# Kernel tuning notes

Measured on AMD Instinct MI355X. Metric: run time of the kernel, lower is better.

The kernel has to match this reference:

```python
import jax, jax.numpy as jnp
import numpy as np

N, E, F, H, L = 100000, 1200000, 64, 64, 4


def setup_inputs() -> dict:
    key = jax.random.key(0)
    ks = jax.random.split(key, 24)
    s = 1.0 / np.sqrt(H)
    x = jax.random.normal(ks[0], (N, F), dtype=jnp.float32)
    edge_index = jax.random.randint(ks[1], (2, E), 0, N, dtype=jnp.int32)
    W1 = jax.random.normal(ks[2], (F, H), jnp.float32) / np.sqrt(F)
    b1 = jnp.zeros((H,), jnp.float32)
    W2 = jax.random.normal(ks[3], (H, H), jnp.float32) * s
    b2 = jnp.zeros((H,), jnp.float32)
    # stacked per-direction (2: fw, bw) per-layer (L) conv params
    def mk(k):
        return jax.random.normal(k, (2, L, H, H), jnp.float32) * s
    gWk, gWq, gWv, gWs = mk(ks[4]), mk(ks[5]), mk(ks[6]), mk(ks[7])
    gbk = jnp.zeros((2, L, H), jnp.float32)
    gbq = jnp.zeros((2, L, H), jnp.float32)
    gbv = jnp.zeros((2, L, H), jnp.float32)
    gb = jnp.zeros((2, L, H), jnp.float32)
    Wsc = jax.random.normal(ks[8], (2 * H, 1), jnp.float32) / np.sqrt(2 * H)
    bsc = jnp.zeros((1,), jnp.float32)
    return dict(x=x, edge_index=edge_index, W1=W1, b1=b1, W2=W2, b2=b2,
                gWk=gWk, gbk=gbk, gWq=gWq, gbq=gbq, gWv=gWv, gbv=gbv,
                gWs=gWs, gb=gb, Wsc=Wsc, bsc=bsc)


def _res_gated_conv(h, src, dst, Wk, bk, Wq, bq, Wv, bv, Ws, b):
    # PyG ResGatedGraphConv: out_i = h_i @ Ws + b + sum_{(j->i)} sigmoid(k_i + q_j) * v_j
    k = h @ Wk + bk            # [N,H]
    q = h @ Wq + bq            # [N,H]
    v = h @ Wv + bv            # [N,H]
    eta = jax.nn.sigmoid(k[dst] + q[src])          # [E,H] per-edge gate
    agg = jax.ops.segment_sum(eta * v[src], dst, num_segments=h.shape[0])
    return agg + h @ Ws + b


def reference(x, edge_index, W1, b1, W2, b2, gWk, gbk, gWq, gbq, gWv, gbv, gWs, gb, Wsc, bsc):
    h = jax.nn.relu(x @ W1 + b1) @ W2 + b2
    src, dst = edge_index[0], edge_index[1]
    # forward direction: messages source -> target (aggregate at dst)
    h_fw = h
    for l in range(L):
        h_fw = _res_gated_conv(h_fw, src, dst, gWk[0, l], gbk[0, l], gWq[0, l], gbq[0, l],
                               gWv[0, l], gbv[0, l], gWs[0, l], gb[0, l])
    # backward direction: flow 'target_to_source' (aggregate at src)
    h_bw = h
    for l in range(L):
        h_bw = _res_gated_conv(h_bw, dst, src, gWk[1, l], gbk[1, l], gWq[1, l], gbq[1, l],
                               gWv[1, l], gbv[1, l], gWs[1, l], gb[1, l])
    score = jnp.concatenate([h_fw, h_bw], axis=1) @ Wsc + bsc
    return score
```

## Files before the change

kernel.cpp:

```cpp
#include <hip/hip_runtime.h>
#include <hip/hip_bf16.h>
#include <hip/hip_fp16.h>


constexpr int HDIM = 64;
constexpr int CAP = 42;
constexpr int NBIN = 2 * (CAP + 1);

union H2U { uint32_t u; __half2 h2; };
union H1U { unsigned short u; __half h; };

typedef _Float16 f16x2 __attribute__((ext_vector_type(2)));
union F2U { uint32_t u; f16x2 h; };

__device__ __forceinline__ float fdot2(f16x2 a, f16x2 b, float c) {
#if __has_builtin(__builtin_amdgcn_fdot2)
    return __builtin_amdgcn_fdot2(a, b, c, false);
#else
    return fmaf((float)a.x, (float)b.x, fmaf((float)a.y, (float)b.y, c));
#endif
}

__global__ __launch_bounds__(256) void mlp_kernel(
    const float* __restrict__ x, const float* __restrict__ W1, const float* __restrict__ b1,
    const float* __restrict__ W2, const float* __restrict__ b2,
    float* __restrict__ hfw, float* __restrict__ hbw, int N, int ntiles)
{
    __shared__ float sW1[64 * 64];
    __shared__ float sW2[64 * 64];
    __shared__ float sb1[64], sb2[64];
    __shared__ float sh[64][36];
    int t = threadIdx.x;
    for (int i = t; i < 1024; i += 256) {
        ((float4*)sW1)[i] = ((const float4*)W1)[i];
        ((float4*)sW2)[i] = ((const float4*)W2)[i];
    }
    if (t < 64) { sb1[t] = b1[t]; sb2[t] = b2[t]; }
    int c = t & 63, rg = t >> 6;

    for (int tile = blockIdx.x; tile < ntiles; tile += gridDim.x) {
        int base = tile * 32;
        __syncthreads();
        for (int i = t; i < 32 * 16; i += 256) {
            int r = i >> 4, fq = i & 15;
            int row = base + r;
            float4 hv = make_float4(0.f, 0.f, 0.f, 0.f);
            if (row < N) hv = ((const float4*)x)[(size_t)row * 16 + fq];
            sh[fq * 4 + 0][r] = hv.x; sh[fq * 4 + 1][r] = hv.y;
            sh[fq * 4 + 2][r] = hv.z; sh[fq * 4 + 3][r] = hv.w;
        }
        __syncthreads();

        float acc[8];
        #pragma unroll
        for (int r = 0; r < 8; r++) acc[r] = sb1[c];
        #pragma unroll 4
        for (int f = 0; f < 64; f++) {
            float w = sW1[f * 64 + c];
            float4 ha = *(const float4*)&sh[f][rg * 8];
            float4 hb = *(const float4*)&sh[f][rg * 8 + 4];
            float hr[8] = {ha.x, ha.y, ha.z, ha.w, hb.x, hb.y, hb.z, hb.w};
            #pragma unroll
            for (int r = 0; r < 8; r++) acc[r] = fmaf(hr[r], w, acc[r]);
        }
        __syncthreads();
        #pragma unroll
        for (int r = 0; r < 8; r++) sh[c][rg * 8 + r] = fmaxf(acc[r], 0.f);
        __syncthreads();

        float acc2[8];
        #pragma unroll
        for (int r = 0; r < 8; r++) acc2[r] = sb2[c];
        #pragma unroll 4
        for (int f = 0; f < 64; f++) {
            float w = sW2[f * 64 + c];
            float4 ha = *(const float4*)&sh[f][rg * 8];
            float4 hb = *(const float4*)&sh[f][rg * 8 + 4];
            float hr[8] = {ha.x, ha.y, ha.z, ha.w, hb.x, hb.y, hb.z, hb.w};
            #pragma unroll
            for (int r = 0; r < 8; r++) acc2[r] = fmaf(hr[r], w, acc2[r]);
        }
        #pragma unroll
        for (int r = 0; r < 8; r++) {
            int row = base + rg * 8 + r;
            if (row < N) {
                hfw[(size_t)row * 64 + c] = acc2[r];
                hbw[(size_t)row * 64 + c] = acc2[r];
            }
        }
    }
}

__global__ __launch_bounds__(256) void expand_kernel(
    const int* __restrict__ srcA, const int* __restrict__ dstA,
    int* __restrict__ cur_fw, int* __restrict__ cur_bw,
    int* __restrict__ col_fw, int* __restrict__ col_bw, int E, int NS)
{
    int slice = blockIdx.x & 7;
    int grank = blockIdx.x >> 3;
    int gb = gridDim.x >> 3;
    int lo = slice * NS, hi = lo + NS;
    int stride = gb * 256;
    for (int e = grank * 256 + threadIdx.x; e < E; e += stride) {
        int s = srcA[e], d = dstA[e];
        if (d >= lo && d < hi) { int c = atomicAdd(&cur_fw[d], 1); if (c < CAP) col_fw[(size_t)d * CAP + c] = s; }
        if (s >= lo && s < hi) { int c = atomicAdd(&cur_bw[s], 1); if (c < CAP) col_bw[(size_t)s * CAP + c] = d; }
    }
}

__global__ __launch_bounds__(256) void dsort_phase1(
    const int* __restrict__ deg_fw, const int* __restrict__ deg_bw,
    int* __restrict__ gcount, int* __restrict__ blockBase, int N)
{
    __shared__ int hist[NBIN];
    int t = threadIdx.x;
    if (t < NBIN) hist[t] = 0;
    __syncthreads();
    int i = blockIdx.x * 256 + t;
    if (i < N) {
        atomicAdd(&hist[min(deg_fw[i], CAP)], 1);
        atomicAdd(&hist[(CAP + 1) + min(deg_bw[i], CAP)], 1);
    }
    __syncthreads();
    if (t < NBIN) {
        int c = hist[t];
        int old = c ? atomicAdd(&gcount[t], c) : 0;
        blockBase[(size_t)blockIdx.x * NBIN + t] = old;
    }
}

__global__ void dsort_phase2(const int* __restrict__ gcount, int* __restrict__ bucketBase)
{
    if (threadIdx.x == 0) {
        int off = 0;
        for (int k = 0; k <= CAP; k++) { bucketBase[k] = off; off += gcount[k]; }
        off = 0;
        for (int k = 0; k <= CAP; k++) { bucketBase[(CAP + 1) + k] = off; off += gcount[(CAP + 1) + k]; }
    }
}

__global__ __launch_bounds__(256) void dsort_phase3(
    const int* __restrict__ deg_fw, const int* __restrict__ deg_bw,
    const int* __restrict__ bucketBase, const int* __restrict__ blockBase,
    int* __restrict__ perm_fw, int* __restrict__ perm_bw, int N)
{
    __shared__ int cur[NBIN];
    int t = threadIdx.x;
    if (t < NBIN) cur[t] = 0;
    __syncthreads();
    int i = blockIdx.x * 256 + t;
    if (i < N) {
        int bf = min(deg_fw[i], CAP);
        int r = atomicAdd(&cur[bf], 1);
        perm_fw[bucketBase[bf] + blockBase[(size_t)blockIdx.x * NBIN + bf] + r] = i;
        int bb = (CAP + 1) + min(deg_bw[i], CAP);
        int r2 = atomicAdd(&cur[bb], 1);
        perm_bw[bucketBase[bb] + blockBase[(size_t)blockIdx.x * NBIN + bb] + r2] = i;
    }
}

__global__ __launch_bounds__(256) void kqvs_kernel(
    const float* h,
    const float* __restrict__ Wk, const float* __restrict__ bk,
    const float* __restrict__ Wq, const float* __restrict__ bq,
    const float* __restrict__ Wv, const float* __restrict__ bv,
    const float* __restrict__ Ws, const float* __restrict__ bs,
    unsigned short* __restrict__ ko, uint32_t* __restrict__ qvo,
    float* oo, int N, int ntiles)
{
    __shared__ f16x2 sW[4][32 * 64];
    __shared__ float sb[4][64];
    __shared__ f16x2 sh[32][34];
    int t = threadIdx.x;
    {
        const float* Wsrc[4] = {Wk, Wq, Wv, Ws};
        #pragma unroll
        for (int m = 0; m < 4; m++) {
            const float* W = Wsrc[m];
            for (int i = t; i < 512; i += 256) {
                int fp = i >> 4, cq = (i & 15) * 4;
                float4 wa = *(const float4*)&W[(size_t)(2 * fp) * 64 + cq];
                float4 wb = *(const float4*)&W[(size_t)(2 * fp + 1) * 64 + cq];
                f16x2 p0 = {(_Float16)wa.x, (_Float16)wb.x};
                f16x2 p1 = {(_Float16)wa.y, (_Float16)wb.y};
                f16x2 p2 = {(_Float16)wa.z, (_Float16)wb.z};
                f16x2 p3 = {(_Float16)wa.w, (_Float16)wb.w};
                sW[m][fp * 64 + cq + 0] = p0;
                sW[m][fp * 64 + cq + 1] = p1;
                sW[m][fp * 64 + cq + 2] = p2;
                sW[m][fp * 64 + cq + 3] = p3;
            }
        }
        if (t < 64) { sb[0][t] = bk[t]; sb[1][t] = bq[t]; sb[2][t] = bv[t]; sb[3][t] = bs[t]; }
    }
    int c = t & 63, rg = t >> 6;

    for (int tile = blockIdx.x; tile < ntiles; tile += gridDim.x) {
        int base = tile * 32;
        __syncthreads();
        for (int i = t; i < 32 * 16; i += 256) {
            int r = i >> 4, fq = i & 15;
            int row = base + r;
            float4 hv = make_float4(0.f, 0.f, 0.f, 0.f);
            if (row < N) hv = ((const float4*)h)[(size_t)row * 16 + fq];
            f16x2 pa = {(_Float16)hv.x, (_Float16)hv.y};
            f16x2 pb = {(_Float16)hv.z, (_Float16)hv.w};
            sh[fq * 2 + 0][r] = pa;
            sh[fq * 2 + 1][r] = pb;
        }
        __syncthreads();

        float acc[8][4];
        #pragma unroll
        for (int r = 0; r < 8; r++) {
            acc[r][0] = sb[0][c]; acc[r][1] = sb[1][c]; acc[r][2] = sb[2][c]; acc[r][3] = sb[3][c];
        }
        #pragma unroll 4
        for (int fp = 0; fp < 32; fp++) {
            f16x2 w0 = sW[0][fp * 64 + c], w1 = sW[1][fp * 64 + c];
            f16x2 w2 = sW[2][fp * 64 + c], w3 = sW[3][fp * 64 + c];
            uint4 A = *(const uint4*)&sh[fp][rg * 8];
            uint4 B = *(const uint4*)&sh[fp][rg * 8 + 4];
            uint32_t hw[8] = {A.x, A.y, A.z, A.w, B.x, B.y, B.z, B.w};
            #pragma unroll
            for (int r = 0; r < 8; r++) {
                F2U hr; hr.u = hw[r];
                acc[r][0] = fdot2(hr.h, w0, acc[r][0]);
                acc[r][1] = fdot2(hr.h, w1, acc[r][1]);
                acc[r][2] = fdot2(hr.h, w2, acc[r][2]);
                acc[r][3] = fdot2(hr.h, w3, acc[r][3]);
            }
        }
        #pragma unroll
        for (int r = 0; r < 8; r++) {
            int row = base + rg * 8 + r;
            if (row < N) {
                size_t o = (size_t)row * 64 + c;
                H1U pk1; pk1.h = __float2half_rn(acc[r][0]);
                ko[o] = pk1.u;
                H2U pk;
                pk.h2.x = __float2half_rn(acc[r][1]);
                pk.h2.y = __float2half_rn(acc[r][2]);
                qvo[o] = pk.u;
                oo[o] = acc[r][3];
            }
        }
    }
}

__device__ __forceinline__ float gate_term(float kd, uint32_t u) {
    H2U c; c.u = u;
    float qf = __low2float(c.h2);
    float vf = __high2float(c.h2);
    float eta = __builtin_amdgcn_rcpf(1.f + __expf(-(kd + qf)));
    return eta * vf;
}

__global__ __launch_bounds__(256) void edge_csr_kernel(
    const int* __restrict__ perm, const int* __restrict__ deg,
    const int* __restrict__ col,
    const uint2* __restrict__ kh2, const uint4* __restrict__ qv4,
    float* h, const float* __restrict__ hother,
    const float* __restrict__ Wsc, const float* __restrict__ bsc,
    float* __restrict__ outp, int do_score, int N)
{
    int t = threadIdx.x;
    int l = t & 15;
    int qd = (t >> 4) & 3;
    int w = (blockIdx.x * 256 + t) >> 6;
    int nw = (gridDim.x * 256) >> 6;
    int nquads = (N + 3) >> 2;
    for (int p = w; p < nquads; p += nw) {
        int task = p * 4 + qd;
        bool act = task < N;
        int i = act ? perm[task] : 0;
        int dg = act ? min(deg[i], CAP) : 0;
        int j = i * CAP, je = j + dg;
        size_t o = (size_t)i * 16 + l;
        uint2 ku = kh2[o];
        H2U k0, k1; k0.u = ku.x; k1.u = ku.y;
        float kd0 = __low2float(k0.h2), kd1 = __high2float(k0.h2);
        float kd2 = __low2float(k1.h2), kd3 = __high2float(k1.h2);
        float4 hold = ((const float4*)h)[o];
        float a0 = 0.f, a1 = 0.f, a2 = 0.f, a3 = 0.f;
        #define GT4(U) { a0 += gate_term(kd0, (U).x); a1 += gate_term(kd1, (U).y); \
                         a2 += gate_term(kd2, (U).z); a3 += gate_term(kd3, (U).w); }
        while (j + 8 <= je) {
            int s0 = col[j + 0], s1 = col[j + 1], s2 = col[j + 2], s3 = col[j + 3];
            int s4 = col[j + 4], s5 = col[j + 5], s6 = col[j + 6], s7 = col[j + 7];
            uint4 u0 = qv4[(size_t)s0 * 16 + l];
            uint4 u1 = qv4[(size_t)s1 * 16 + l];
            uint4 u2 = qv4[(size_t)s2 * 16 + l];
            uint4 u3 = qv4[(size_t)s3 * 16 + l];
            uint4 u4 = qv4[(size_t)s4 * 16 + l];
            uint4 u5 = qv4[(size_t)s5 * 16 + l];
            uint4 u6 = qv4[(size_t)s6 * 16 + l];
            uint4 u7 = qv4[(size_t)s7 * 16 + l];
            GT4(u0); GT4(u1); GT4(u2); GT4(u3);
            GT4(u4); GT4(u5); GT4(u6); GT4(u7);
            j += 8;
        }
        if (j + 4 <= je) {
            int s0 = col[j + 0], s1 = col[j + 1], s2 = col[j + 2], s3 = col[j + 3];
            uint4 u0 = qv4[(size_t)s0 * 16 + l];
            uint4 u1 = qv4[(size_t)s1 * 16 + l];
            uint4 u2 = qv4[(size_t)s2 * 16 + l];
            uint4 u3 = qv4[(size_t)s3 * 16 + l];
            GT4(u0); GT4(u1); GT4(u2); GT4(u3);
            j += 4;
        }
        while (j < je) {
            int s0 = col[j];
            uint4 u0 = qv4[(size_t)s0 * 16 + l];
            GT4(u0);
            ++j;
        }
        #undef GT4
        float4 nh = make_float4(a0 + hold.x, a1 + hold.y, a2 + hold.z, a3 + hold.w);
        if (act) ((float4*)h)[o] = nh;
        if (do_score) {
            float4 hf = make_float4(0.f, 0.f, 0.f, 0.f);
            if (act) hf = ((const float4*)hother)[o];
            const float4 wf = ((const float4*)Wsc)[l];
            const float4 wb = ((const float4*)Wsc)[16 + l];
            float pp = hf.x * wf.x + hf.y * wf.y + hf.z * wf.z + hf.w * wf.w
                     + nh.x * wb.x + nh.y * wb.y + nh.z * wb.z + nh.w * wb.w;
            #pragma unroll
            for (int off = 8; off; off >>= 1) pp += __shfl_xor(pp, off, 64);
            if (act && l == 0) outp[i] = pp + bsc[0];
        }
    }
}

extern "C" void kernel_launch(void* const* d_in, const int* in_sizes, int n_in,
                              void* d_out, int out_size, void* d_ws, size_t ws_size,
                              hipStream_t stream)
{
    const float* x   = (const float*)d_in[0];
    const int*   ei  = (const int*)d_in[1];
    const float* W1  = (const float*)d_in[2];
    const float* b1  = (const float*)d_in[3];
    const float* W2  = (const float*)d_in[4];
    const float* b2  = (const float*)d_in[5];
    const float* gWk = (const float*)d_in[6];
    const float* gbk = (const float*)d_in[7];
    const float* gWq = (const float*)d_in[8];
    const float* gbq = (const float*)d_in[9];
    const float* gWv = (const float*)d_in[10];
    const float* gbv = (const float*)d_in[11];
    const float* gWs = (const float*)d_in[12];
    const float* gb  = (const float*)d_in[13];
    const float* Wsc = (const float*)d_in[14];
    const float* bsc = (const float*)d_in[15];

    const int N = in_sizes[0] / HDIM;
    const int E = in_sizes[1] / 2;
    const int L = 4;
    const int NS = (N + 7) / 8;
    int nb = (N + 255) / 256;
    int ntiles = (N + 31) / 32;

    size_t N64 = (size_t)N * HDIM;
    size_t Npad = (size_t)N + 64;
    float* ws    = (float*)d_ws;
    float* h_fw  = ws;
    float* h_bw  = ws + N64;
    uint32_t* qvbuf = (uint32_t*)(ws + 2 * N64);
    unsigned short* kbuf = (unsigned short*)(ws + 3 * N64);
    int* cur_fw  = (int*)(ws + 3 * N64 + N64 / 2);
    int* cur_bw  = cur_fw + Npad;
    int* gcount  = cur_bw + Npad;
    int* bucketBase = gcount + 128;
    int* perm_fw = bucketBase + 128;
    int* perm_bw = perm_fw + N;
    int* blockBase = perm_bw + N;
    int* col_fw  = blockBase + (size_t)nb * NBIN;
    int* col_bw  = col_fw + (size_t)N * CAP;

    const int* srcA = ei;
    const int* dstA = ei + E;

    mlp_kernel<<<768, 256, 0, stream>>>(x, W1, b1, W2, b2, h_fw, h_bw, N, ntiles);

    hipMemsetAsync(cur_fw, 0, (2 * Npad + 128) * sizeof(int), stream);
    expand_kernel<<<2048, 256, 0, stream>>>(srcA, dstA, cur_fw, cur_bw, col_fw, col_bw, E, NS);
    dsort_phase1<<<nb, 256, 0, stream>>>(cur_fw, cur_bw, gcount, blockBase, N);
    dsort_phase2<<<1, 64, 0, stream>>>(gcount, bucketBase);
    dsort_phase3<<<nb, 256, 0, stream>>>(cur_fw, cur_bw, bucketBase, blockBase,
                                         perm_fw, perm_bw, N);

    for (int dir = 0; dir < 2; dir++) {
        float* h = dir ? h_bw : h_fw;
        float* hother = dir ? h_fw : h_bw;
        const int* perm = dir ? perm_bw : perm_fw;
        const int* deg  = dir ? cur_bw : cur_fw;
        const int* col  = dir ? col_bw : col_fw;
        for (int l = 0; l < L; l++) {
            int off = dir * L + l;
            int do_score = (dir == 1 && l == L - 1) ? 1 : 0;
            kqvs_kernel<<<1024, 256, 0, stream>>>(h,
                gWk + (size_t)off * 4096, gbk + (size_t)off * 64,
                gWq + (size_t)off * 4096, gbq + (size_t)off * 64,
                gWv + (size_t)off * 4096, gbv + (size_t)off * 64,
                gWs + (size_t)off * 4096, gb  + (size_t)off * 64,
                kbuf, qvbuf, h, N, ntiles);
            edge_csr_kernel<<<2048, 256, 0, stream>>>(perm, deg, col,
                (const uint2*)kbuf, (const uint4*)qvbuf, h, hother,
                Wsc, bsc, (float*)d_out, do_score, N);
        }
    }
}
```

Before: 931.5 us.

## Build padded CSR through a bucketed counting sort instead of global atomics

Replaces the single expand kernel, which does per-edge global atomicAdd on degree counters and scattered writes into the padded adjacency, with a four-stage bucket sort. Edges are counted and scattered into 256-node range buckets using shared-memory histograms, then each range is filled into a shared-memory window and written out contiguously along with its degrees. This removes contended global atomics and random global writes, at the cost of extra passes over the edge list and an intermediate bucket buffer that reuses the qv workspace. The single-thread serial scan over roughly 800 buckets and 43 KB of shared memory per fill block may limit occupancy.

```diff
diff --git a/kernel.cpp b/kernel.cpp
--- a/kernel.cpp
+++ b/kernel.cpp
@@ -6,6 +6,7 @@
 constexpr int HDIM = 64;
 constexpr int CAP = 42;
 constexpr int NBIN = 2 * (CAP + 1);
+constexpr int RANGE = 256;
 
 union H2U { uint32_t u; __half2 h2; };
 union H1U { unsigned short u; __half h; };
@@ -91,21 +92,86 @@
     }
 }
 
-__global__ __launch_bounds__(256) void expand_kernel(
+__global__ __launch_bounds__(256) void bexp_count(
     const int* __restrict__ srcA, const int* __restrict__ dstA,
-    int* __restrict__ cur_fw, int* __restrict__ cur_bw,
-    int* __restrict__ col_fw, int* __restrict__ col_bw, int E, int NS)
-{
-    int slice = blockIdx.x & 7;
-    int grank = blockIdx.x >> 3;
-    int gb = gridDim.x >> 3;
-    int lo = slice * NS, hi = lo + NS;
-    int stride = gb * 256;
-    for (int e = grank * 256 + threadIdx.x; e < E; e += stride) {
+    int* __restrict__ gcount, int* __restrict__ blockBase, int E, int NR)
+{
+    extern __shared__ int hist[];
+    int nb2 = 2 * NR;
+    for (int i = threadIdx.x; i < nb2; i += 256) hist[i] = 0;
+    __syncthreads();
+    int stride = gridDim.x * 256;
+    for (int e = blockIdx.x * 256 + threadIdx.x; e < E; e += stride) {
         int s = srcA[e], d = dstA[e];
-        if (d >= lo && d < hi) { int c = atomicAdd(&cur_fw[d], 1); if (c < CAP) col_fw[(size_t)d * CAP + c] = s; }
-        if (s >= lo && s < hi) { int c = atomicAdd(&cur_bw[s], 1); if (c < CAP) col_bw[(size_t)s * CAP + c] = d; }
-    }
+        atomicAdd(&hist[d >> 8], 1);
+        atomicAdd(&hist[NR + (s >> 8)], 1);
+    }
+    __syncthreads();
+    for (int i = threadIdx.x; i < nb2; i += 256) {
+        int c = hist[i];
+        blockBase[(size_t)blockIdx.x * nb2 + i] = c ? atomicAdd(&gcount[i], c) : 0;
+    }
+}
+
+__global__ void bexp_scan(const int* __restrict__ gcount, int* __restrict__ bucketBase, int nb2)
+{
+    if (threadIdx.x == 0) {
+        int off = 0;
+        for (int k = 0; k < nb2; k++) { bucketBase[k] = off; off += gcount[k]; }
+    }
+}
+
+__global__ __launch_bounds__(256) void bexp_scatter(
+    const int* __restrict__ srcA, const int* __restrict__ dstA,
+    const int* __restrict__ bucketBase, const int* __restrict__ blockBase,
+    uint2* __restrict__ bucket, int E, int NR)
+{
+    extern __shared__ int cur[];
+    int nb2 = 2 * NR;
+    for (int i = threadIdx.x; i < nb2; i += 256) cur[i] = 0;
+    __syncthreads();
+    int stride = gridDim.x * 256;
+    const int* bb = blockBase + (size_t)blockIdx.x * nb2;
+    for (int e = blockIdx.x * 256 + threadIdx.x; e < E; e += stride) {
+        int s = srcA[e], d = dstA[e];
+        int bf = d >> 8;
+        int r = atomicAdd(&cur[bf], 1);
+        bucket[bucketBase[bf] + bb[bf] + r] = make_uint2((unsigned)d, (unsigned)s);
+        int bw = NR + (s >> 8);
+        int r2 = atomicAdd(&cur[bw], 1);
+        bucket[bucketBase[bw] + bb[bw] + r2] = make_uint2((unsigned)s, (unsigned)d);
+    }
+}
+
+__global__ __launch_bounds__(256) void bexp_fill(
+    const uint2* __restrict__ bucket, const int* __restrict__ gcount,
+    const int* __restrict__ bucketBase,
+    int* __restrict__ col_fw, int* __restrict__ col_bw,
+    int* __restrict__ deg_fw, int* __restrict__ deg_bw, int N, int NR)
+{
+    __shared__ int cnt[RANGE];
+    __shared__ int win[RANGE * CAP];
+    int blk = blockIdx.x;
+    int dir = blk >= NR;
+    int r = dir ? blk - NR : blk;
+    int lo = r * RANGE;
+    int nnode = min(RANGE, N - lo);
+    if (nnode <= 0) return;
+    for (int i = threadIdx.x; i < RANGE; i += 256) cnt[i] = 0;
+    __syncthreads();
+    int base = bucketBase[blk], tot = gcount[blk];
+    for (int i = threadIdx.x; i < tot; i += 256) {
+        uint2 en = bucket[base + i];
+        int li = (int)en.x - lo;
+        int c = atomicAdd(&cnt[li], 1);
+        if (c < CAP) win[li * CAP + c] = (int)en.y;
+    }
+    __syncthreads();
+    int* col = dir ? col_bw : col_fw;
+    int* deg = dir ? deg_bw : deg_fw;
+    int total = nnode * CAP;
+    for (int i = threadIdx.x; i < total; i += 256) col[(size_t)lo * CAP + i] = win[i];
+    for (int i = threadIdx.x; i < nnode; i += 256) deg[lo + i] = cnt[i];
 }
 
 __global__ __launch_bounds__(256) void dsort_phase1(
@@ -356,7 +422,8 @@
     const int N = in_sizes[0] / HDIM;
     const int E = in_sizes[1] / 2;
     const int L = 4;
-    const int NS = (N + 7) / 8;
+    const int NR = (N + RANGE - 1) / RANGE;
+    const int nb2 = 2 * NR;
     int nb = (N + 255) / 256;
     int ntiles = (N + 31) / 32;
 
@@ -367,33 +434,42 @@
     float* h_bw  = ws + N64;
     uint32_t* qvbuf = (uint32_t*)(ws + 2 * N64);
     unsigned short* kbuf = (unsigned short*)(ws + 3 * N64);
-    int* cur_fw  = (int*)(ws + 3 * N64 + N64 / 2);
-    int* cur_bw  = cur_fw + Npad;
-    int* gcount  = cur_bw + Npad;
-    int* bucketBase = gcount + 128;
-    int* perm_fw = bucketBase + 128;
+    int* deg_fw  = (int*)(ws + 3 * N64 + N64 / 2);
+    int* deg_bw  = deg_fw + Npad;
+    int* gcountE = deg_bw + Npad;
+    int* bucketBaseE = gcountE + 1024;
+    int* gcountD = bucketBaseE + 1024;
+    int* bucketBaseD = gcountD + 128;
+    int* blockBase = bucketBaseD + 128;
+    int* perm_fw = blockBase + 128 * 1024;
     int* perm_bw = perm_fw + N;
-    int* blockBase = perm_bw + N;
-    int* col_fw  = blockBase + (size_t)nb * NBIN;
+    int* col_fw  = perm_bw + N;
     int* col_bw  = col_fw + (size_t)N * CAP;
+    uint2* bucket = (uint2*)qvbuf;
 
     const int* srcA = ei;
     const int* dstA = ei + E;
 
     mlp_kernel<<<768, 256, 0, stream>>>(x, W1, b1, W2, b2, h_fw, h_bw, N, ntiles);
 
-    hipMemsetAsync(cur_fw, 0, (2 * Npad + 128) * sizeof(int), stream);
-    expand_kernel<<<2048, 256, 0, stream>>>(srcA, dstA, cur_fw, cur_bw, col_fw, col_bw, E, NS);
-    dsort_phase1<<<nb, 256, 0, stream>>>(cur_fw, cur_bw, gcount, blockBase, N);
-    dsort_phase2<<<1, 64, 0, stream>>>(gcount, bucketBase);
-    dsort_phase3<<<nb, 256, 0, stream>>>(cur_fw, cur_bw, bucketBase, blockBase,
+    hipMemsetAsync(gcountE, 0, (1024 + 1024 + 128 + 128) * sizeof(int), stream);
+    bexp_count<<<128, 256, nb2 * sizeof(int), stream>>>(srcA, dstA, gcountE, blockBase, E, NR);
+    bexp_scan<<<1, 64, 0, stream>>>(gcountE, bucketBaseE, nb2);
+    bexp_scatter<<<128, 256, nb2 * sizeof(int), stream>>>(srcA, dstA, bucketBaseE, blockBase,
+                                                          bucket, E, NR);
+    bexp_fill<<<nb2, 256, 0, stream>>>(bucket, gcountE, bucketBaseE,
+                                       col_fw, col_bw, deg_fw, deg_bw, N, NR);
+
+    dsort_phase1<<<nb, 256, 0, stream>>>(deg_fw, deg_bw, gcountD, blockBase, N);
+    dsort_phase2<<<1, 64, 0, stream>>>(gcountD, bucketBaseD);
+    dsort_phase3<<<nb, 256, 0, stream>>>(deg_fw, deg_bw, bucketBaseD, blockBase,
                                          perm_fw, perm_bw, N);
 
     for (int dir = 0; dir < 2; dir++) {
         float* h = dir ? h_bw : h_fw;
         float* hother = dir ? h_fw : h_bw;
         const int* perm = dir ? perm_bw : perm_fw;
-        const int* deg  = dir ? cur_bw : cur_fw;
+        const int* deg  = dir ? deg_bw : deg_fw;
         const int* col  = dir ? col_bw : col_fw;
         for (int l = 0; l < L; l++) {
             int off = dir * L + l;
```

Measured after the change: 917.2 us. Within noise of the previous version (-1.5%).
